# Optimization experiments

Measured on AMD Instinct MI355X. Metric: run time of the kernel, lower is better.

## Reference

```python
import jax, jax.numpy as jnp
import numpy as np

N = 10000      # num_nodes
E = 320000     # num_edges (before self loops)
F_IN = 256     # num_features
H = 128        # hidden_channels
C = 2          # num_classes
NEG_SLOPE = 0.2  # PyG GATConv default leaky_relu slope


def setup_inputs() -> dict:
    key = jax.random.key(0)
    ks = jax.random.split(key, 12)
    x = jax.random.normal(ks[0], (N, F_IN), dtype=jnp.float32)
    edge_index = jax.random.randint(ks[1], (2, E), 0, N, dtype=jnp.int32)
    s = 0.05
    return {
        "x": x,
        "edge_index": edge_index,
        # GATConv layer 1 (heads=1): lin (no bias), att_src, att_dst, bias
        "W1": jax.random.normal(ks[2], (F_IN, H), dtype=jnp.float32) * s,
        "att_src1": jax.random.normal(ks[3], (H,), dtype=jnp.float32) * s,
        "att_dst1": jax.random.normal(ks[4], (H,), dtype=jnp.float32) * s,
        "b1": jnp.zeros((H,), dtype=jnp.float32),
        # GATConv layer 2
        "W2": jax.random.normal(ks[5], (H, H), dtype=jnp.float32) * s,
        "att_src2": jax.random.normal(ks[6], (H,), dtype=jnp.float32) * s,
        "att_dst2": jax.random.normal(ks[7], (H,), dtype=jnp.float32) * s,
        "b2": jnp.zeros((H,), dtype=jnp.float32),
        # reduce_dim: Linear(H, 1)
        "Wr": jax.random.normal(ks[8], (H, 1), dtype=jnp.float32) * s,
        "br": jnp.zeros((1,), dtype=jnp.float32),
        # classifier: Linear(N, C)
        "Wc": jax.random.normal(ks[9], (N, C), dtype=jnp.float32) * s,
        "bc": jnp.zeros((C,), dtype=jnp.float32),
    }


def _gat_conv(x, src, dst, W, att_src, att_dst, bias):
    """PyG GATConv, heads=1, add_self_loops=True. src/dst include self loops."""
    h = x @ W                           # [N, H]
    a_s = h @ att_src                   # [N]
    a_d = h @ att_dst                   # [N]
    e = a_s[src] + a_d[dst]             # [Etot]
    e = jnp.where(e > 0, e, NEG_SLOPE * e)  # leaky_relu
    # segment softmax over edges grouped by destination node
    m = jax.ops.segment_max(e, dst, num_segments=N)          # [N]
    ex = jnp.exp(e - m[dst])
    z = jax.ops.segment_sum(ex, dst, num_segments=N)         # [N]
    alpha = ex / z[dst]                                       # [Etot]
    out = jax.ops.segment_sum(alpha[:, None] * h[src], dst, num_segments=N)
    return out + bias


def reference(x, edge_index, W1, att_src1, att_dst1, b1,
              W2, att_src2, att_dst2, b2, Wr, br, Wc, bc):
    # add self loops (PyG GATConv default)
    loops = jnp.arange(N, dtype=edge_index.dtype)
    src = jnp.concatenate([edge_index[0], loops])
    dst = jnp.concatenate([edge_index[1], loops])

    h = _gat_conv(x, src, dst, W1, att_src1, att_dst1, b1)
    h = jax.nn.relu(h)
    # dropout(p=0.5) is identity in eval mode
    h = _gat_conv(h, src, dst, W2, att_src2, att_dst2, b2)
    h = jax.nn.relu(h)
    h = h @ Wr + br                     # [N, 1]
    h = h.reshape(1, -1)                # [1, N]
    return h @ Wc + bc                  # [1, C]
```

## Files before the change

kernel.cpp:

```cpp
#include <hip/hip_runtime.h>
#include <hip/hip_bf16.h>

#define NN 10000
#define EE 320000
#define ET (EE + NN)
#define FIN 256
#define HD 128
#define NEG 0.2f



__global__ void k_zero_i(int* __restrict__ p, int n) {
    int i = blockIdx.x * blockDim.x + threadIdx.x;
    if (i < n) p[i] = 0;
}

__global__ void k_hist(const int* __restrict__ ei, int* __restrict__ counts) {
    int i = blockIdx.x * blockDim.x + threadIdx.x;
    if (i >= ET) return;
    int d = (i < EE) ? ei[EE + i] : (i - EE);
    atomicAdd(&counts[d], 1);
}

__global__ void k_scan(const int* __restrict__ counts,
                       int* __restrict__ offsets,
                       int* __restrict__ cursor) {
    const int CHUNK = 40;
    __shared__ int sums[256];
    int t = threadIdx.x;
    int base = t * CHUNK;
    int s = 0;
    for (int i = 0; i < CHUNK; i++) {
        int idx = base + i;
        if (idx < NN) s += counts[idx];
    }
    sums[t] = s;
    __syncthreads();
    for (int off = 1; off < 256; off <<= 1) {
        int v = (t >= off) ? sums[t - off] : 0;
        __syncthreads();
        sums[t] += v;
        __syncthreads();
    }
    int run = (t > 0) ? sums[t - 1] : 0;
    for (int i = 0; i < CHUNK; i++) {
        int idx = base + i;
        if (idx < NN) {
            offsets[idx] = run;
            cursor[idx]  = run;
            run += counts[idx];
        }
    }
    if (t == 255) offsets[NN] = sums[255];
}

__global__ void k_scatter(const int* __restrict__ ei, int* __restrict__ cursor,
                          int* __restrict__ srclist) {
    int i = blockIdx.x * blockDim.x + threadIdx.x;
    if (i >= ET) return;
    int s, d;
    if (i < EE) { s = ei[i]; d = ei[EE + i]; }
    else        { s = i - EE; d = s; }
    int pos = atomicAdd(&cursor[d], 1);
    srclist[pos] = s;
}


__global__ void k_gemm1(const float* __restrict__ x,
                        const float* __restrict__ W,
                        const float* __restrict__ atts,
                        const float* __restrict__ attd,
                        float* __restrict__ h,
                        float* __restrict__ a_s,
                        float* __restrict__ a_d) {
    __shared__ float xs[8 * FIN];
    __shared__ float red[4];
    int t = threadIdx.x;
    int m0 = blockIdx.x * 8;
    const float4* xv = (const float4*)(x + (size_t)m0 * FIN);
    float4* xsv = (float4*)xs;
    #pragma unroll
    for (int i = 0; i < 4; i++)
        xsv[t + 128 * i] = xv[t + 128 * i];
    __syncthreads();

    float acc[8] = {0.f,0.f,0.f,0.f,0.f,0.f,0.f,0.f};
    for (int k = 0; k < FIN; k += 4) {
        float w0 = W[(k + 0) * HD + t];
        float w1 = W[(k + 1) * HD + t];
        float w2 = W[(k + 2) * HD + t];
        float w3 = W[(k + 3) * HD + t];
        #pragma unroll
        for (int m = 0; m < 8; m++) {
            float4 xk = *(const float4*)&xs[m * FIN + k];
            acc[m] += xk.x * w0;
            acc[m] += xk.y * w1;
            acc[m] += xk.z * w2;
            acc[m] += xk.w * w3;
        }
    }

    float at_s = atts[t], at_d = attd[t];
    int lane = t & 63, wid = t >> 6;
    #pragma unroll
    for (int m = 0; m < 8; m++) {
        h[(size_t)(m0 + m) * HD + t] = acc[m];
        float vs = acc[m] * at_s, vd = acc[m] * at_d;
        #pragma unroll
        for (int off = 32; off > 0; off >>= 1) {
            vs += __shfl_down(vs, off);
            vd += __shfl_down(vd, off);
        }
        if (lane == 0) { red[wid] = vs; red[2 + wid] = vd; }
        __syncthreads();
        if (t == 0) {
            a_s[m0 + m] = red[0] + red[1];
            a_d[m0 + m] = red[2] + red[3];
        }
        __syncthreads();
    }
}


__global__ void k_gemm2(const float* __restrict__ x,
                        const float* __restrict__ W,
                        const float* __restrict__ atts,
                        const float* __restrict__ attd,
                        float* __restrict__ h,
                        float* __restrict__ a_s,
                        float* __restrict__ a_d) {
    __shared__ float xs[8 * HD];
    __shared__ float red[4];
    int t = threadIdx.x;
    int m0 = blockIdx.x * 8;
    const float4* xv = (const float4*)(x + (size_t)m0 * HD);
    float4* xsv = (float4*)xs;
    #pragma unroll
    for (int i = 0; i < 2; i++)
        xsv[t + 128 * i] = xv[t + 128 * i];
    __syncthreads();

    float acc[8] = {0.f,0.f,0.f,0.f,0.f,0.f,0.f,0.f};
    for (int k = 0; k < HD; k += 4) {
        float w0 = W[(k + 0) * HD + t];
        float w1 = W[(k + 1) * HD + t];
        float w2 = W[(k + 2) * HD + t];
        float w3 = W[(k + 3) * HD + t];
        #pragma unroll
        for (int m = 0; m < 8; m++) {
            float4 xk = *(const float4*)&xs[m * HD + k];
            acc[m] += xk.x * w0;
            acc[m] += xk.y * w1;
            acc[m] += xk.z * w2;
            acc[m] += xk.w * w3;
        }
    }

    float at_s = atts[t], at_d = attd[t];
    int lane = t & 63, wid = t >> 6;
    #pragma unroll
    for (int m = 0; m < 8; m++) {
        h[(size_t)(m0 + m) * HD + t] = acc[m];
        float vs = acc[m] * at_s, vd = acc[m] * at_d;
        #pragma unroll
        for (int off = 32; off > 0; off >>= 1) {
            vs += __shfl_down(vs, off);
            vd += __shfl_down(vd, off);
        }
        if (lane == 0) { red[wid] = vs; red[2 + wid] = vd; }
        __syncthreads();
        if (t == 0) {
            a_s[m0 + m] = red[0] + red[1];
            a_d[m0 + m] = red[2] + red[3];
        }
        __syncthreads();
    }
}


__device__ __forceinline__ float edge_exp(float as_v, float adn) {
    float e = as_v + adn;
    e = (e > 0.f) ? e : NEG * e;
    return expf(e);
}

__global__ void k_agg1(const int* __restrict__ offsets,
                       const int* __restrict__ srclist,
                       const float* __restrict__ a_s,
                       const float* __restrict__ a_d,
                       const float* __restrict__ h,
                       const float* __restrict__ bias,
                       float* __restrict__ g) {
    int node = blockIdx.x;
    int t = threadIdx.x;
    int beg = offsets[node], end = offsets[node + 1];
    float adn = a_d[node];
    float acc = 0.f, z = 0.f;
    int p = beg;
    for (; p + 4 <= end; p += 4) {
        int s0 = srclist[p], s1 = srclist[p + 1], s2 = srclist[p + 2], s3 = srclist[p + 3];
        float h0 = h[(size_t)s0 * HD + t];
        float h1 = h[(size_t)s1 * HD + t];
        float h2 = h[(size_t)s2 * HD + t];
        float h3 = h[(size_t)s3 * HD + t];
        float x0 = edge_exp(a_s[s0], adn);
        float x1 = edge_exp(a_s[s1], adn);
        float x2 = edge_exp(a_s[s2], adn);
        float x3 = edge_exp(a_s[s3], adn);
        z += x0 + x1 + x2 + x3;
        acc += x0 * h0 + x1 * h1 + x2 * h2 + x3 * h3;
    }
    for (; p < end; p++) {
        int s = srclist[p];
        float hv = h[(size_t)s * HD + t];
        float ex = edge_exp(a_s[s], adn);
        z += ex;
        acc += ex * hv;
    }
    float o = acc / z + bias[t];
    g[(size_t)node * HD + t] = (o > 0.f) ? o : 0.f;
}

__global__ void k_agg2(const int* __restrict__ offsets,
                       const int* __restrict__ srclist,
                       const float* __restrict__ a_s,
                       const float* __restrict__ a_d,
                       const float* __restrict__ h,
                       const float* __restrict__ bias,
                       const float* __restrict__ Wr,
                       const float* __restrict__ br,
                       float* __restrict__ r) {
    __shared__ float red[128];
    int node = blockIdx.x;
    int t = threadIdx.x;
    int beg = offsets[node], end = offsets[node + 1];
    float adn = a_d[node];
    float acc = 0.f, z = 0.f;
    int p = beg;
    for (; p + 4 <= end; p += 4) {
        int s0 = srclist[p], s1 = srclist[p + 1], s2 = srclist[p + 2], s3 = srclist[p + 3];
        float h0 = h[(size_t)s0 * HD + t];
        float h1 = h[(size_t)s1 * HD + t];
        float h2 = h[(size_t)s2 * HD + t];
        float h3 = h[(size_t)s3 * HD + t];
        float x0 = edge_exp(a_s[s0], adn);
        float x1 = edge_exp(a_s[s1], adn);
        float x2 = edge_exp(a_s[s2], adn);
        float x3 = edge_exp(a_s[s3], adn);
        z += x0 + x1 + x2 + x3;
        acc += x0 * h0 + x1 * h1 + x2 * h2 + x3 * h3;
    }
    for (; p < end; p++) {
        int s = srclist[p];
        float hv = h[(size_t)s * HD + t];
        float ex = edge_exp(a_s[s], adn);
        z += ex;
        acc += ex * hv;
    }
    float o = acc / z + bias[t];
    o = (o > 0.f) ? o : 0.f;
    red[t] = o * Wr[t];
    __syncthreads();
    for (int off = 64; off > 0; off >>= 1) {
        if (t < off) red[t] += red[t + off];
        __syncthreads();
    }
    if (t == 0) r[node] = red[0] + br[0];
}


__global__ void k_cls(const float* __restrict__ r,
                      const float* __restrict__ Wc,
                      const float* __restrict__ bc,
                      float* __restrict__ out) {
    __shared__ float r0[256], r1[256];
    int t = threadIdx.x;
    float c0 = 0.f, c1 = 0.f;
    for (int n = t; n < NN; n += 256) {
        float rv = r[n];
        c0 += rv * Wc[2 * n];
        c1 += rv * Wc[2 * n + 1];
    }
    r0[t] = c0; r1[t] = c1;
    __syncthreads();
    for (int off = 128; off > 0; off >>= 1) {
        if (t < off) { r0[t] += r0[t + off]; r1[t] += r1[t + off]; }
        __syncthreads();
    }
    if (t == 0) {
        out[0] = r0[0] + bc[0];
        out[1] = r1[0] + bc[1];
    }
}


extern "C" void kernel_launch(void* const* d_in, const int* in_sizes, int n_in,
                              void* d_out, int out_size, void* d_ws, size_t ws_size,
                              hipStream_t stream) {
    const float* x    = (const float*)d_in[0];
    const int*   ei   = (const int*)d_in[1];
    const float* W1   = (const float*)d_in[2];
    const float* as1  = (const float*)d_in[3];
    const float* ad1  = (const float*)d_in[4];
    const float* b1   = (const float*)d_in[5];
    const float* W2   = (const float*)d_in[6];
    const float* as2  = (const float*)d_in[7];
    const float* ad2  = (const float*)d_in[8];
    const float* b2   = (const float*)d_in[9];
    const float* Wr   = (const float*)d_in[10];
    const float* br   = (const float*)d_in[11];
    const float* Wc   = (const float*)d_in[12];
    const float* bc   = (const float*)d_in[13];
    float* out = (float*)d_out;

    float* h    = (float*)d_ws;
    float* g1   = h + (size_t)NN * HD;
    float* a_s  = g1 + (size_t)NN * HD;
    float* a_d  = a_s + NN;
    float* r    = a_d + NN;
    int* counts  = (int*)(r + NN);
    int* offsets = counts + NN;
    int* cursor  = offsets + NN + 1;
    int* srclist = cursor + NN;

    const int TPB = 256;
    const int gET = (ET + TPB - 1) / TPB;
    const int gNN = (NN + TPB - 1) / TPB;

    k_zero_i<<<gNN, TPB, 0, stream>>>(counts, NN);
    k_hist<<<gET, TPB, 0, stream>>>(ei, counts);
    k_scan<<<1, 256, 0, stream>>>(counts, offsets, cursor);
    k_scatter<<<gET, TPB, 0, stream>>>(ei, cursor, srclist);

    k_gemm1<<<NN / 8, 128, 0, stream>>>(x, W1, as1, ad1, h, a_s, a_d);
    k_agg1<<<NN, 128, 0, stream>>>(offsets, srclist, a_s, a_d, h, b1, g1);

    k_gemm2<<<NN / 8, 128, 0, stream>>>(g1, W2, as2, ad2, h, a_s, a_d);
    k_agg2<<<NN, 128, 0, stream>>>(offsets, srclist, a_s, a_d, h, b2, Wr, br, r);

    k_cls<<<1, 256, 0, stream>>>(r, Wc, bc, out);
}
```

Baseline: 266.3 us.

## Split aggregation edges across four sub-warps with float4 gathers; restructure GEMM per-wave

The aggregation kernels now assign each 32-thread slot a strided subset of a node's incoming edges. Each thread gathers a float4 of the source feature row, and the four partial sums are combined through shared memory. This gives more independent memory requests in flight per block and wider loads, at the cost of one extra shared-memory reduction. The GEMM kernels process 16 rows per block, each wavefront owns 8 rows and two output columns per thread. That removes the per-row __syncthreads attention reduction and replaces it with wave-only shuffles. expf is swapped for the faster __expf intrinsic, which is slightly less precise.

```diff
diff --git a/kernel.cpp b/kernel.cpp
--- a/kernel.cpp
+++ b/kernel.cpp
@@ -73,51 +73,54 @@
                         float* __restrict__ h,
                         float* __restrict__ a_s,
                         float* __restrict__ a_d) {
-    __shared__ float xs[8 * FIN];
-    __shared__ float red[4];
-    int t = threadIdx.x;
-    int m0 = blockIdx.x * 8;
+    __shared__ float xs[16 * FIN];
+    int t = threadIdx.x;
+    int m0 = blockIdx.x * 16;
     const float4* xv = (const float4*)(x + (size_t)m0 * FIN);
     float4* xsv = (float4*)xs;
     #pragma unroll
-    for (int i = 0; i < 4; i++)
+    for (int i = 0; i < 8; i++)
         xsv[t + 128 * i] = xv[t + 128 * i];
     __syncthreads();
 
-    float acc[8] = {0.f,0.f,0.f,0.f,0.f,0.f,0.f,0.f};
+    int g = t >> 6;
+    int tt = t & 63;
+    int f = tt * 2;
+    const float* xg = xs + g * 8 * FIN;
+
+    float2 acc[8];
+    #pragma unroll
+    for (int m = 0; m < 8; m++) acc[m] = make_float2(0.f, 0.f);
+
     for (int k = 0; k < FIN; k += 4) {
-        float w0 = W[(k + 0) * HD + t];
-        float w1 = W[(k + 1) * HD + t];
-        float w2 = W[(k + 2) * HD + t];
-        float w3 = W[(k + 3) * HD + t];
+        float2 w0 = *(const float2*)&W[(k + 0) * HD + f];
+        float2 w1 = *(const float2*)&W[(k + 1) * HD + f];
+        float2 w2 = *(const float2*)&W[(k + 2) * HD + f];
+        float2 w3 = *(const float2*)&W[(k + 3) * HD + f];
         #pragma unroll
         for (int m = 0; m < 8; m++) {
-            float4 xk = *(const float4*)&xs[m * FIN + k];
-            acc[m] += xk.x * w0;
-            acc[m] += xk.y * w1;
-            acc[m] += xk.z * w2;
-            acc[m] += xk.w * w3;
-        }
-    }
-
-    float at_s = atts[t], at_d = attd[t];
-    int lane = t & 63, wid = t >> 6;
+            float4 xk = *(const float4*)&xg[m * FIN + k];
+            acc[m].x += xk.x * w0.x; acc[m].y += xk.x * w0.y;
+            acc[m].x += xk.y * w1.x; acc[m].y += xk.y * w1.y;
+            acc[m].x += xk.z * w2.x; acc[m].y += xk.z * w2.y;
+            acc[m].x += xk.w * w3.x; acc[m].y += xk.w * w3.y;
+        }
+    }
+
+    float2 ats = *(const float2*)&atts[f];
+    float2 atd = *(const float2*)&attd[f];
     #pragma unroll
     for (int m = 0; m < 8; m++) {
-        h[(size_t)(m0 + m) * HD + t] = acc[m];
-        float vs = acc[m] * at_s, vd = acc[m] * at_d;
+        int node = m0 + g * 8 + m;
+        *(float2*)&h[(size_t)node * HD + f] = acc[m];
+        float vs = acc[m].x * ats.x + acc[m].y * ats.y;
+        float vd = acc[m].x * atd.x + acc[m].y * atd.y;
         #pragma unroll
         for (int off = 32; off > 0; off >>= 1) {
             vs += __shfl_down(vs, off);
             vd += __shfl_down(vd, off);
         }
-        if (lane == 0) { red[wid] = vs; red[2 + wid] = vd; }
-        __syncthreads();
-        if (t == 0) {
-            a_s[m0 + m] = red[0] + red[1];
-            a_d[m0 + m] = red[2] + red[3];
-        }
-        __syncthreads();
+        if (tt == 0) { a_s[node] = vs; a_d[node] = vd; }
     }
 }
 
@@ -129,95 +132,108 @@
                         float* __restrict__ h,
                         float* __restrict__ a_s,
                         float* __restrict__ a_d) {
-    __shared__ float xs[8 * HD];
-    __shared__ float red[4];
-    int t = threadIdx.x;
-    int m0 = blockIdx.x * 8;
+    __shared__ float xs[16 * HD];
+    int t = threadIdx.x;
+    int m0 = blockIdx.x * 16;
     const float4* xv = (const float4*)(x + (size_t)m0 * HD);
     float4* xsv = (float4*)xs;
     #pragma unroll
-    for (int i = 0; i < 2; i++)
+    for (int i = 0; i < 4; i++)
         xsv[t + 128 * i] = xv[t + 128 * i];
     __syncthreads();
 
-    float acc[8] = {0.f,0.f,0.f,0.f,0.f,0.f,0.f,0.f};
+    int g = t >> 6;
+    int tt = t & 63;
+    int f = tt * 2;
+    const float* xg = xs + g * 8 * HD;
+
+    float2 acc[8];
+    #pragma unroll
+    for (int m = 0; m < 8; m++) acc[m] = make_float2(0.f, 0.f);
+
     for (int k = 0; k < HD; k += 4) {
-        float w0 = W[(k + 0) * HD + t];
-        float w1 = W[(k + 1) * HD + t];
-        float w2 = W[(k + 2) * HD + t];
-        float w3 = W[(k + 3) * HD + t];
+        float2 w0 = *(const float2*)&W[(k + 0) * HD + f];
+        float2 w1 = *(const float2*)&W[(k + 1) * HD + f];
+        float2 w2 = *(const float2*)&W[(k + 2) * HD + f];
+        float2 w3 = *(const float2*)&W[(k + 3) * HD + f];
         #pragma unroll
         for (int m = 0; m < 8; m++) {
-            float4 xk = *(const float4*)&xs[m * HD + k];
-            acc[m] += xk.x * w0;
-            acc[m] += xk.y * w1;
-            acc[m] += xk.z * w2;
-            acc[m] += xk.w * w3;
-        }
-    }
-
-    float at_s = atts[t], at_d = attd[t];
-    int lane = t & 63, wid = t >> 6;
+            float4 xk = *(const float4*)&xg[m * HD + k];
+            acc[m].x += xk.x * w0.x; acc[m].y += xk.x * w0.y;
+            acc[m].x += xk.y * w1.x; acc[m].y += xk.y * w1.y;
+            acc[m].x += xk.z * w2.x; acc[m].y += xk.z * w2.y;
+            acc[m].x += xk.w * w3.x; acc[m].y += xk.w * w3.y;
+        }
+    }
+
+    float2 ats = *(const float2*)&atts[f];
+    float2 atd = *(const float2*)&attd[f];
     #pragma unroll
     for (int m = 0; m < 8; m++) {
-        h[(size_t)(m0 + m) * HD + t] = acc[m];
-        float vs = acc[m] * at_s, vd = acc[m] * at_d;
+        int node = m0 + g * 8 + m;
+        *(float2*)&h[(size_t)node * HD + f] = acc[m];
+        float vs = acc[m].x * ats.x + acc[m].y * ats.y;
+        float vd = acc[m].x * atd.x + acc[m].y * atd.y;
         #pragma unroll
         for (int off = 32; off > 0; off >>= 1) {
             vs += __shfl_down(vs, off);
             vd += __shfl_down(vd, off);
         }
-        if (lane == 0) { red[wid] = vs; red[2 + wid] = vd; }
-        __syncthreads();
-        if (t == 0) {
-            a_s[m0 + m] = red[0] + red[1];
-            a_d[m0 + m] = red[2] + red[3];
-        }
-        __syncthreads();
-    }
-}
-
-
-__device__ __forceinline__ float edge_exp(float as_v, float adn) {
+        if (tt == 0) { a_s[node] = vs; a_d[node] = vd; }
+    }
+}
+
+
+__device__ __forceinline__ float edge_w(float as_v, float adn) {
     float e = as_v + adn;
     e = (e > 0.f) ? e : NEG * e;
-    return expf(e);
+    return __expf(e);
 }
 
 __global__ void k_agg1(const int* __restrict__ offsets,
                        const int* __restrict__ srclist,
                        const float* __restrict__ a_s,
                        const float* __restrict__ a_d,
-                       const float* __restrict__ h,
+                       const float4* __restrict__ h4,
                        const float* __restrict__ bias,
                        float* __restrict__ g) {
+    __shared__ float accs[4][HD];
+    __shared__ float zs[4];
     int node = blockIdx.x;
     int t = threadIdx.x;
+    int slot = t >> 5, q = t & 31;
     int beg = offsets[node], end = offsets[node + 1];
     float adn = a_d[node];
-    float acc = 0.f, z = 0.f;
-    int p = beg;
-    for (; p + 4 <= end; p += 4) {
-        int s0 = srclist[p], s1 = srclist[p + 1], s2 = srclist[p + 2], s3 = srclist[p + 3];
-        float h0 = h[(size_t)s0 * HD + t];
-        float h1 = h[(size_t)s1 * HD + t];
-        float h2 = h[(size_t)s2 * HD + t];
-        float h3 = h[(size_t)s3 * HD + t];
-        float x0 = edge_exp(a_s[s0], adn);
-        float x1 = edge_exp(a_s[s1], adn);
-        float x2 = edge_exp(a_s[s2], adn);
-        float x3 = edge_exp(a_s[s3], adn);
-        z += x0 + x1 + x2 + x3;
-        acc += x0 * h0 + x1 * h1 + x2 * h2 + x3 * h3;
-    }
-    for (; p < end; p++) {
-        int s = srclist[p];
-        float hv = h[(size_t)s * HD + t];
-        float ex = edge_exp(a_s[s], adn);
-        z += ex;
-        acc += ex * hv;
-    }
-    float o = acc / z + bias[t];
+    float4 acc = make_float4(0.f, 0.f, 0.f, 0.f);
+    float z = 0.f;
+    int p = beg + slot;
+    for (; p + 4 < end; p += 8) {
+        int s0 = srclist[p];
+        int s1 = srclist[p + 4];
+        float4 h0 = h4[(size_t)s0 * 32 + q];
+        float4 h1 = h4[(size_t)s1 * 32 + q];
+        float w0 = edge_w(a_s[s0], adn);
+        float w1 = edge_w(a_s[s1], adn);
+        z += w0 + w1;
+        acc.x += w0 * h0.x + w1 * h1.x;
+        acc.y += w0 * h0.y + w1 * h1.y;
+        acc.z += w0 * h0.z + w1 * h1.z;
+        acc.w += w0 * h0.w + w1 * h1.w;
+    }
+    if (p < end) {
+        int s0 = srclist[p];
+        float4 h0 = h4[(size_t)s0 * 32 + q];
+        float w0 = edge_w(a_s[s0], adn);
+        z += w0;
+        acc.x += w0 * h0.x; acc.y += w0 * h0.y;
+        acc.z += w0 * h0.z; acc.w += w0 * h0.w;
+    }
+    *(float4*)&accs[slot][q * 4] = acc;
+    if (q == 0) zs[slot] = z;
+    __syncthreads();
+    float v = accs[0][t] + accs[1][t] + accs[2][t] + accs[3][t];
+    float zz = zs[0] + zs[1] + zs[2] + zs[3];
+    float o = v / zz + bias[t];
     g[(size_t)node * HD + t] = (o > 0.f) ? o : 0.f;
 }
 
@@ -225,47 +241,56 @@
                        const int* __restrict__ srclist,
                        const float* __restrict__ a_s,
                        const float* __restrict__ a_d,
-                       const float* __restrict__ h,
+                       const float4* __restrict__ h4,
                        const float* __restrict__ bias,
                        const float* __restrict__ Wr,
                        const float* __restrict__ br,
                        float* __restrict__ r) {
-    __shared__ float red[128];
+    __shared__ float accs[4][HD];
+    __shared__ float zs[4];
+    __shared__ float red[2];
     int node = blockIdx.x;
     int t = threadIdx.x;
+    int slot = t >> 5, q = t & 31;
     int beg = offsets[node], end = offsets[node + 1];
     float adn = a_d[node];
-    float acc = 0.f, z = 0.f;
-    int p = beg;
-    for (; p + 4 <= end; p += 4) {
-        int s0 = srclist[p], s1 = srclist[p + 1], s2 = srclist[p + 2], s3 = srclist[p + 3];
-        float h0 = h[(size_t)s0 * HD + t];
-        float h1 = h[(size_t)s1 * HD + t];
-        float h2 = h[(size_t)s2 * HD + t];
-        float h3 = h[(size_t)s3 * HD + t];
-        float x0 = edge_exp(a_s[s0], adn);
-        float x1 = edge_exp(a_s[s1], adn);
-        float x2 = edge_exp(a_s[s2], adn);
-        float x3 = edge_exp(a_s[s3], adn);
-        z += x0 + x1 + x2 + x3;
-        acc += x0 * h0 + x1 * h1 + x2 * h2 + x3 * h3;
-    }
-    for (; p < end; p++) {
-        int s = srclist[p];
-        float hv = h[(size_t)s * HD + t];
-        float ex = edge_exp(a_s[s], adn);
-        z += ex;
-        acc += ex * hv;
-    }
-    float o = acc / z + bias[t];
+    float4 acc = make_float4(0.f, 0.f, 0.f, 0.f);
+    float z = 0.f;
+    int p = beg + slot;
+    for (; p + 4 < end; p += 8) {
+        int s0 = srclist[p];
+        int s1 = srclist[p + 4];
+        float4 h0 = h4[(size_t)s0 * 32 + q];
+        float4 h1 = h4[(size_t)s1 * 32 + q];
+        float w0 = edge_w(a_s[s0], adn);
+        float w1 = edge_w(a_s[s1], adn);
+        z += w0 + w1;
+        acc.x += w0 * h0.x + w1 * h1.x;
+        acc.y += w0 * h0.y + w1 * h1.y;
+        acc.z += w0 * h0.z + w1 * h1.z;
+        acc.w += w0 * h0.w + w1 * h1.w;
+    }
+    if (p < end) {
+        int s0 = srclist[p];
+        float4 h0 = h4[(size_t)s0 * 32 + q];
+        float w0 = edge_w(a_s[s0], adn);
+        z += w0;
+        acc.x += w0 * h0.x; acc.y += w0 * h0.y;
+        acc.z += w0 * h0.z; acc.w += w0 * h0.w;
+    }
+    *(float4*)&accs[slot][q * 4] = acc;
+    if (q == 0) zs[slot] = z;
+    __syncthreads();
+    float v = accs[0][t] + accs[1][t] + accs[2][t] + accs[3][t];
+    float zz = zs[0] + zs[1] + zs[2] + zs[3];
+    float o = v / zz + bias[t];
     o = (o > 0.f) ? o : 0.f;
-    red[t] = o * Wr[t];
-    __syncthreads();
-    for (int off = 64; off > 0; off >>= 1) {
-        if (t < off) red[t] += red[t + off];
-        __syncthreads();
-    }
-    if (t == 0) r[node] = red[0] + br[0];
+    float part = o * Wr[t];
+    #pragma unroll
+    for (int off = 32; off > 0; off >>= 1) part += __shfl_down(part, off);
+    if ((t & 63) == 0) red[t >> 6] = part;
+    __syncthreads();
+    if (t == 0) r[node] = red[0] + red[1] + br[0];
 }
 
 
@@ -332,11 +357,11 @@
     k_scan<<<1, 256, 0, stream>>>(counts, offsets, cursor);
     k_scatter<<<gET, TPB, 0, stream>>>(ei, cursor, srclist);
 
-    k_gemm1<<<NN / 8, 128, 0, stream>>>(x, W1, as1, ad1, h, a_s, a_d);
-    k_agg1<<<NN, 128, 0, stream>>>(offsets, srclist, a_s, a_d, h, b1, g1);
-
-    k_gemm2<<<NN / 8, 128, 0, stream>>>(g1, W2, as2, ad2, h, a_s, a_d);
-    k_agg2<<<NN, 128, 0, stream>>>(offsets, srclist, a_s, a_d, h, b2, Wr, br, r);
+    k_gemm1<<<NN / 16, 128, 0, stream>>>(x, W1, as1, ad1, h, a_s, a_d);
+    k_agg1<<<NN, 128, 0, stream>>>(offsets, srclist, a_s, a_d, (const float4*)h, b1, g1);
+
+    k_gemm2<<<NN / 16, 128, 0, stream>>>(g1, W2, as2, ad2, h, a_s, a_d);
+    k_agg2<<<NN, 128, 0, stream>>>(offsets, srclist, a_s, a_d, (const float4*)h, b2, Wr, br, r);
 
     k_cls<<<1, 256, 0, stream>>>(r, Wc, bc, out);
 }
```

New measurement: 249.9 us. -6.1%, faster.
